# Kernel optimization log

Measured on AMD Instinct MI355X. Metric: run time of the kernel, lower is better.

The kernel has to match this reference:

```python
import jax, jax.numpy as jnp
import numpy as np

# structural constants (from dg config / init_kwargs)
B = 8192      # batch (L=1)
N = 64        # number of columns
C = 16        # one-hot width per column
D = N * C     # 1024
NUM = 32      # first NUM columns are numeric (use info['range'])
NCAUSAL = 16  # causal_cols = range(16)
K = 8         # info['range'][i] is [C, K]
HS = 1024
HP = 1024
TAU = 0.7
SMOOTH = 0.1  # kwargs['smoothing']


def setup_inputs() -> dict:
    key = jax.random.key(0)
    ks = jax.random.split(key, 20)
    s = 0.02
    inp = {
        'x': jax.random.uniform(ks[0], (B, D), dtype=jnp.float32),
        'truth_x': jax.random.normal(ks[1], (B, N), dtype=jnp.float32),
        # selector: Linear(D,HS) -> ReLU -> Linear(HS,N) -> Sigmoid
        'sel_w1': jax.random.normal(ks[2], (D, HS)) * s,
        'sel_b1': jnp.zeros((HS,), jnp.float32),
        'sel_w2': jax.random.normal(ks[3], (HS, N)) * s,
        'sel_b2': jnp.zeros((N,), jnp.float32),
        # perturber: D->HP->HP->HP->D with ReLU between
        'pw1': jax.random.normal(ks[4], (D, HP)) * s,
        'pb1': jnp.zeros((HP,), jnp.float32),
        'pw2': jax.random.normal(ks[5], (HP, HP)) * s,
        'pb2': jnp.zeros((HP,), jnp.float32),
        'pw3': jax.random.normal(ks[6], (HP, HP)) * s,
        'pb3': jnp.zeros((HP,), jnp.float32),
        'pw4': jax.random.normal(ks[7], (HP, D)) * s,
        'pb4': jnp.zeros((D,), jnp.float32),
        # dg.info['range'][i] for numeric columns: [NUM, C, K]
        'ranges': jax.random.normal(ks[8], (NUM, C, K), dtype=jnp.float32),
        # pre-drawn noise (training branch)
        'unif_a': jax.random.uniform(ks[9], (B, N), minval=1e-6, maxval=1.0 - 1e-6),
        'unif_b': jax.random.uniform(ks[10], (B, N), minval=1e-6, maxval=1.0 - 1e-6),
        'gumbel': jax.random.gumbel(ks[11], (B, N, C), dtype=jnp.float32),
    }
    return inp


def reference(x, truth_x, sel_w1, sel_b1, sel_w2, sel_b2,
              pw1, pb1, pw2, pb2, pw3, pb3, pw4, pb4,
              ranges, unif_a, unif_b, gumbel):
    # selector -> P in (0,1), shape [B, N]
    P = jax.nn.sigmoid(jax.nn.relu(x @ sel_w1 + sel_b1) @ sel_w2 + sel_b2)
    # relaxed Bernoulli (Sample_Bernoulli, training branch)
    ga = -jnp.log(-jnp.log(unif_a))
    gb = -jnp.log(-jnp.log(unif_b))
    no_logits = P * jnp.exp(ga) / TAU
    de_logits = no_logits + (1.0 - P) * jnp.exp(gb) / TAU
    probs = no_logits / de_logits                       # [B, N]
    # perturber MLP -> W, shape [B, D]
    h = jax.nn.relu(x @ pw1 + pb1)
    h = jax.nn.relu(h @ pw2 + pb2)
    h = jax.nn.relu(h @ pw3 + pb3)
    W = h @ pw4 + pb4
    # per-column blocks
    xr = x.reshape(B, N, C)
    logits = W.reshape(B, N, C)
    # data-dependent causal masking for causal columns
    curr = jnp.argmax(xr, axis=-1)                      # [B, N]
    causal = (jnp.arange(N) < NCAUSAL)[None, :, None]   # [1, N, 1]
    below = jnp.arange(C)[None, None, :] < curr[:, :, None]
    mask = jnp.where(causal & below, -100.0, jnp.where(causal, 1.0, 0.0))
    logits = logits + mask
    # label smoothing then Gumbel-softmax (soft), per Sample_Categorical
    pr = jax.nn.softmax(logits, axis=-1)
    pr = (1.0 - SMOOTH) * pr + SMOOTH / C
    logits = jnp.log(pr)
    y = jax.nn.softmax((logits + gumbel) / TAU, axis=-1)  # [B, N, C]
    # numeric columns: map categorical sample through range table, mix with truth
    xt_num = jnp.einsum('bnc,nck->bnk', y[:, :NUM], ranges).mean(axis=-1)  # [B, NUM]
    p_num = probs[:, :NUM]
    out_num = p_num * xt_num + (1.0 - p_num) * truth_x[:, :NUM]           # [B, NUM]
    # categorical columns: mix relaxed sample with original one-hot block
    p_cat = probs[:, NUM:, None]
    out_cat = p_cat * y[:, NUM:] + (1.0 - p_cat) * xr[:, NUM:]            # [B, N-NUM, C]
    xcf = jnp.concatenate([out_num, out_cat.reshape(B, (N - NUM) * C)], axis=1)
    return truth_x, xcf, P, W
```

## Files before the change

### kernel.cpp

```cpp
#include <hip/hip_runtime.h>
#include <hip/hip_bf16.h>
#include <cstdint>

#define B_DIM 8192
#define N_DIM 64
#define C_DIM 16
#define D_DIM 1024
#define NUM 32
#define NCAUSAL 16
#define K_RANGES 8
#define HS 1024
#define HP 1024
#define TAU 0.7f
#define SMOOTH 0.1f

typedef __bf16 bf16x8 __attribute__((ext_vector_type(8)));
typedef float f32x16 __attribute__((ext_vector_type(16)));

typedef const __attribute__((address_space(1))) uint32_t* gas_ptr;
typedef __attribute__((address_space(3))) uint32_t* las_ptr;

__device__ __forceinline__ void gld_lds16(const void* g, void* l) {
    __builtin_amdgcn_global_load_lds((gas_ptr)(uintptr_t)g,
                                     (las_ptr)(uint32_t)(uintptr_t)l,
                                     16, 0, 0);
}

__device__ __forceinline__ int swz(int r) { return (r & 3) ^ ((r >> 2) & 3); }

__device__ __forceinline__ void xcd_remap(int& bx, int& by)
{
    int gx  = gridDim.x;
    int nwg = gx * gridDim.y;
    int lin = by * gx + bx;
    int cpx = nwg >> 3;
    int sw  = (lin & 7) * cpx + (lin >> 3);
    by = sw / gx;
    bx = sw - by * gx;
}

template <int ACT>
__device__ __forceinline__ void gemm_body8(
    const ushort* __restrict__ Ag, const ushort* __restrict__ Bg,
    const float* __restrict__ bias,
    float* __restrict__ Cf, __hip_bfloat16* __restrict__ Cb,
    int lda, int Nout, int ldC, int K, long m0, long n0,
    uint4 (*As)[512], uint4 (*Bs)[512], f32x16* accExp = nullptr)
{
    const int tid  = threadIdx.x;
    const int wave = tid >> 6;
    const int ln31 = tid & 31, blk = (tid >> 5) & 1;
    const int wr = wave >> 2, wc = wave & 3;

    const int row = tid >> 2;
    const int ch  = (tid & 3) ^ swz(row);
    const ushort* aSrc = Ag + (m0 + row) * (long)lda + ch * 8;
    const ushort* bSrc = Bg + (n0 + row) * (long)K   + ch * 8;
    const int ldsOff = wave << 6;

    f32x16 acc[2];
    acc[0] = (f32x16)(0.0f);
    acc[1] = (f32x16)(0.0f);

#define ISSUE_STAGE8(buf, kt)                                                  \
    {                                                                          \
        gld_lds16(aSrc + (kt), &As[buf][ldsOff]);                              \
        gld_lds16(bSrc + (kt), &Bs[buf][ldsOff]);                              \
    }

    const int nt = K >> 5;
    ISSUE_STAGE8(0, 0);
    ISSUE_STAGE8(1, 32);

    int rb = 0;
    for (int t = 0; t < nt; ++t) {
        if (t < nt - 1) {
            asm volatile("s_waitcnt vmcnt(2)" ::: "memory");
        } else {
            asm volatile("s_waitcnt vmcnt(0)" ::: "memory");
        }
        __builtin_amdgcn_s_barrier();

        if (t + 2 < nt) {
            int sb = rb + 2; if (sb >= 3) sb -= 3;
            ISSUE_STAGE8(sb, (t + 2) * 32);
        }

        bf16x8 af[2][2], bfr[2];
#pragma unroll
        for (int ks = 0; ks < 2; ++ks) {
            int c = ks * 2 + blk;
#pragma unroll
            for (int mi = 0; mi < 2; ++mi) {
                int r = wr * 64 + mi * 32 + ln31;
                af[ks][mi] = __builtin_bit_cast(bf16x8, As[rb][r * 4 + (c ^ swz(r))]);
            }
            int n = wc * 32 + ln31;
            bfr[ks] = __builtin_bit_cast(bf16x8, Bs[rb][n * 4 + (c ^ swz(n))]);
        }
#pragma unroll
        for (int ks = 0; ks < 2; ++ks)
#pragma unroll
            for (int mi = 0; mi < 2; ++mi)
                acc[mi] = __builtin_amdgcn_mfma_f32_32x32x16_bf16(
                    af[ks][mi], bfr[ks], acc[mi], 0, 0, 0);

        rb = (rb == 2) ? 0 : rb + 1;
    }
#undef ISSUE_STAGE8

    if (ACT == 3) { accExp[0] = acc[0]; accExp[1] = acc[1]; }

    long col = n0 + wc * 32 + ln31;
    if (col < Nout) {
        float bs = bias ? bias[col] : 0.0f;
#pragma unroll
        for (int mi = 0; mi < 2; ++mi) {
#pragma unroll
            for (int reg = 0; reg < 16; ++reg) {
                long r2 = m0 + wr * 64 + mi * 32 + (reg & 3) + 8 * (reg >> 2) + 4 * blk;
                float v = acc[mi][reg] + bs;
                if (ACT == 1) {
                    v = fmaxf(v, 0.0f);
                    Cb[r2 * (long)ldC + col] = __float2bfloat16(v);
                } else if (ACT == 2) {
                    v = 1.0f / (1.0f + __expf(-v));
                    Cf[r2 * (long)ldC + col] = v;
                } else {
                    Cf[r2 * (long)ldC + col] = v;
                }
            }
        }
    }
}

template <int ACT>
__global__ __launch_bounds__(512, 4) void gemm8(
    const __hip_bfloat16* __restrict__ A, const __hip_bfloat16* __restrict__ Bt,
    const float* __restrict__ bias,
    float* __restrict__ Cf, __hip_bfloat16* __restrict__ Cb,
    int lda, int Nout, int ldC, int K)
{
    __shared__ uint4 As[3][512];
    __shared__ uint4 Bs[3][512];
    int bx = blockIdx.x, by = blockIdx.y;
    xcd_remap(bx, by);
    gemm_body8<ACT>((const ushort*)A, (const ushort*)Bt, bias, Cf, Cb,
                    lda, Nout, ldC, K,
                    (long)by * 128, (long)bx * 128, As, Bs);
}

__global__ __launch_bounds__(512, 4) void gemm8_fused23(
    const __hip_bfloat16* __restrict__ act1,
    const __hip_bfloat16* __restrict__ p2t, const float* __restrict__ pb2,
    __hip_bfloat16* __restrict__ actB,
    const __hip_bfloat16* __restrict__ w2t, const float* __restrict__ sel_b2,
    float* __restrict__ outP)
{
    __shared__ uint4 As[3][512];
    __shared__ uint4 Bs[3][512];
    int bx = blockIdx.x, by = blockIdx.y;
    xcd_remap(bx, by);
    long m0 = (long)by * 128;
    if (bx < 8) {
        gemm_body8<1>((const ushort*)(act1 + 1024), (const ushort*)p2t, pb2,
                      nullptr, actB, 2048, 1024, 1024, 1024,
                      m0, (long)bx * 128, As, Bs);
    } else {
        gemm_body8<2>((const ushort*)act1, (const ushort*)w2t, sel_b2,
                      outP, nullptr, 2048, 64, 64, 1024,
                      m0, 0, As, Bs);
    }
}

struct FinArgs {
    const float* x; const float* truth; const float* ua; const float* ub;
    const float* gum; const float* rmean; const float* P;
    float* out_truth; float* out_xcf;
};

__global__ __launch_bounds__(512, 4) void gemm8_final(
    const __hip_bfloat16* __restrict__ A, const __hip_bfloat16* __restrict__ Bt,
    const float* __restrict__ bias, float* __restrict__ W,
    int lda, int K, FinArgs fa)
{
    __shared__ uint4 smem[3072];
    uint4 (*As)[512] = reinterpret_cast<uint4(*)[512]>(smem);
    uint4 (*Bs)[512] = reinterpret_cast<uint4(*)[512]>(smem + 1536);

    int bx = blockIdx.x, by = blockIdx.y;
    xcd_remap(bx, by);
    const long m0 = (long)by * 128;
    const long n0 = (long)bx * 128;

    f32x16 accE[2];
    gemm_body8<3>((const ushort*)A, (const ushort*)Bt, bias, W, nullptr,
                  lda, 1024, 1024, K, m0, n0, As, Bs, accE);

    const int tid  = threadIdx.x;
    const int wave = tid >> 6;
    const int ln31 = tid & 31, blk = (tid >> 5) & 1;
    const int wr = wave >> 2, wc = wave & 3;

    float* tile = (float*)smem;
    const float bs = bias[n0 + wc * 32 + ln31];

    const int lb = tid >> 3;
    const int ng = tid & 7;
    const int n  = (int)(n0 >> 4) + ng;

    for (int h = 0; h < 2; ++h) {
        __syncthreads();
        if (wr == h) {
#pragma unroll
            for (int mi = 0; mi < 2; ++mi)
#pragma unroll
                for (int reg = 0; reg < 16; ++reg) {
                    int lr = mi * 32 + (reg & 3) + 8 * (reg >> 2) + 4 * blk;
                    tile[lr * 132 + wc * 32 + ln31] = accE[mi][reg] + bs;
                }
        }
        __syncthreads();

        long b   = m0 + h * 64 + lb;
        long idx = b * 64 + n;

        float tx = fa.truth[idx];
        fa.out_truth[idx] = tx;

        float p  = fa.P[idx];
        float ea = -1.0f / logf(fa.ua[idx]);
        float eb = -1.0f / logf(fa.ub[idx]);
        float no = p * ea;
        float probs = no / (no + (1.0f - p) * eb);

        const float* Wrow = tile + lb * 132 + ng * 16;
        const float* grow = fa.gum + (size_t)idx * 16;
        float lo[16], g[16], xv[16];
#pragma unroll
        for (int c = 0; c < 16; c += 4) {
            float4 v = *(const float4*)(Wrow + c);
            lo[c] = v.x; lo[c + 1] = v.y; lo[c + 2] = v.z; lo[c + 3] = v.w;
            float4 gv = *(const float4*)(grow + c);
            g[c] = gv.x; g[c + 1] = gv.y; g[c + 2] = gv.z; g[c + 3] = gv.w;
        }

        bool needx = (n < NCAUSAL) || (n >= NUM);
        if (needx) {
            const float* xrow = fa.x + (size_t)idx * 16;
#pragma unroll
            for (int c = 0; c < 16; c += 4) {
                float4 v = *(const float4*)(xrow + c);
                xv[c] = v.x; xv[c + 1] = v.y; xv[c + 2] = v.z; xv[c + 3] = v.w;
            }
        }

        if (n < NCAUSAL) {
            int curr = 0; float best = xv[0];
#pragma unroll
            for (int c = 1; c < 16; ++c)
                if (xv[c] > best) { best = xv[c]; curr = c; }
#pragma unroll
            for (int c = 0; c < 16; ++c) lo[c] += (c < curr) ? -100.0f : 1.0f;
        }

        float mx = lo[0];
#pragma unroll
        for (int c = 1; c < 16; ++c) mx = fmaxf(mx, lo[c]);
        float s = 0.0f, pr[16];
#pragma unroll
        for (int c = 0; c < 16; ++c) { pr[c] = __expf(lo[c] - mx); s += pr[c]; }
        float inv = 1.0f / s;
#pragma unroll
        for (int c = 0; c < 16; ++c)
            pr[c] = (1.0f - SMOOTH) * pr[c] * inv + (SMOOTH / C_DIM);

        float t[16];
        float mx2 = -1e30f;
#pragma unroll
        for (int c = 0; c < 16; ++c) {
            t[c] = (__logf(pr[c]) + g[c]) * (1.0f / TAU);
            mx2 = fmaxf(mx2, t[c]);
        }
        float s2 = 0.0f;
#pragma unroll
        for (int c = 0; c < 16; ++c) { t[c] = __expf(t[c] - mx2); s2 += t[c]; }
        float inv2 = 1.0f / s2;

        if (n < NUM) {
            float xt = 0.0f;
#pragma unroll
            for (int c = 0; c < 16; ++c) xt += t[c] * inv2 * fa.rmean[n * 16 + c];
            fa.out_xcf[(size_t)b * 544 + n] = probs * xt + (1.0f - probs) * tx;
        } else {
            float* o = fa.out_xcf + (size_t)b * 544 + 32 + (size_t)(n - NUM) * 16;
#pragma unroll
            for (int c = 0; c < 16; ++c)
                o[c] = probs * t[c] * inv2 + (1.0f - probs) * xv[c];
        }
    }
}

struct PrepArgs {
    const float* src[6];
    __hip_bfloat16* dst[6];
    int Nsrc[6];
    int Npad[6];
    const float* ranges; float* rmean;
    const float* b1; const float* b2; float* bcat;
    const float* x; __hip_bfloat16* xbf;
};

__global__ void prep_kernel(PrepArgs a)
{
    int z = blockIdx.z;
    int tx = threadIdx.x, ty = threadIdx.y;
    int t = ty * 32 + tx;
    if (z == 7) {
        int bid = blockIdx.y * 32 + blockIdx.x;
        const float4* s4 = (const float4*)a.x;
        for (int i = bid * 256 + t; i < B_DIM * D_DIM / 4; i += 1024 * 256) {
            float4 v = s4[i];
            __hip_bfloat16* d = a.xbf + (size_t)i * 4;
            d[0] = __float2bfloat16(v.x);
            d[1] = __float2bfloat16(v.y);
            d[2] = __float2bfloat16(v.z);
            d[3] = __float2bfloat16(v.w);
        }
        return;
    }
    if (z == 6) {
        if (blockIdx.x || blockIdx.y) return;
        for (int j = t; j < NUM * C_DIM; j += 256) {
            float s = 0.0f;
#pragma unroll
            for (int k = 0; k < K_RANGES; ++k) s += a.ranges[j * K_RANGES + k];
            a.rmean[j] = s * (1.0f / K_RANGES);
        }
        for (int j = t; j < 1024; j += 256) {
            a.bcat[j]        = a.b1[j];
            a.bcat[1024 + j] = a.b2[j];
        }
        return;
    }
    const int Nsrc = a.Nsrc[z], Npad = a.Npad[z];
    int n0 = blockIdx.x * 32, k0 = blockIdx.y * 32;
    if (n0 >= Npad) return;
    const float* src = a.src[z];
    __hip_bfloat16* dst = a.dst[z];
    __shared__ float tile[32][33];
#pragma unroll
    for (int i = 0; i < 32; i += 8) {
        int k = k0 + ty + i, n = n0 + tx;
        tile[ty + i][tx] = (n < Nsrc) ? src[(size_t)k * Nsrc + n] : 0.0f;
    }
    __syncthreads();
#pragma unroll
    for (int i = 0; i < 32; i += 8) {
        int n = n0 + ty + i, k = k0 + tx;
        dst[(size_t)n * D_DIM + k] = __float2bfloat16(tile[tx][ty + i]);
    }
}

extern "C" void kernel_launch(void* const* d_in, const int* in_sizes, int n_in,
                              void* d_out, int out_size, void* d_ws, size_t ws_size,
                              hipStream_t stream)
{
    const float* x      = (const float*)d_in[0];
    const float* truth  = (const float*)d_in[1];
    const float* sel_w1 = (const float*)d_in[2];
    const float* sel_b1 = (const float*)d_in[3];
    const float* sel_w2 = (const float*)d_in[4];
    const float* sel_b2 = (const float*)d_in[5];
    const float* pw1    = (const float*)d_in[6];
    const float* pb1    = (const float*)d_in[7];
    const float* pw2    = (const float*)d_in[8];
    const float* pb2    = (const float*)d_in[9];
    const float* pw3    = (const float*)d_in[10];
    const float* pb3    = (const float*)d_in[11];
    const float* pw4    = (const float*)d_in[12];
    const float* pb4    = (const float*)d_in[13];
    const float* ranges = (const float*)d_in[14];
    const float* ua     = (const float*)d_in[15];
    const float* ub     = (const float*)d_in[16];
    const float* gum    = (const float*)d_in[17];

    float* out       = (float*)d_out;
    float* out_truth = out;
    float* out_xcf   = out + 524288;
    float* out_P     = out + 4980736;
    float* out_W     = out + 5505024;

    char* w = (char*)d_ws;
    size_t off = 0;
    __hip_bfloat16* A0   = (__hip_bfloat16*)(w + off); off += (size_t)B_DIM * D_DIM * 2;
    __hip_bfloat16* act1 = (__hip_bfloat16*)(w + off); off += (size_t)B_DIM * 2048 * 2;
    __hip_bfloat16* actB = (__hip_bfloat16*)(w + off); off += (size_t)B_DIM * HP * 2;
    __hip_bfloat16* actC = (__hip_bfloat16*)(w + off); off += (size_t)B_DIM * HP * 2;
    __hip_bfloat16* Wcat = (__hip_bfloat16*)(w + off); off += (size_t)2048 * D_DIM * 2;
    __hip_bfloat16* w2t  = (__hip_bfloat16*)(w + off); off += (size_t)128 * HS * 2;
    __hip_bfloat16* p2t  = (__hip_bfloat16*)(w + off); off += (size_t)HP * HP * 2;
    __hip_bfloat16* p3t  = (__hip_bfloat16*)(w + off); off += (size_t)HP * HP * 2;
    __hip_bfloat16* p4t  = (__hip_bfloat16*)(w + off); off += (size_t)D_DIM * HP * 2;
    float* rmean         = (float*)(w + off);          off += 512 * 4;
    float* bcat          = (float*)(w + off);          off += 2048 * 4;
    if (ws_size < off) return;

    PrepArgs pa;
    pa.src[0] = sel_w1; pa.dst[0] = Wcat;               pa.Nsrc[0] = HS;    pa.Npad[0] = 1024;
    pa.src[1] = pw1;    pa.dst[1] = Wcat + 1024 * 1024; pa.Nsrc[1] = HP;    pa.Npad[1] = 1024;
    pa.src[2] = sel_w2; pa.dst[2] = w2t;                pa.Nsrc[2] = N_DIM; pa.Npad[2] = 128;
    pa.src[3] = pw2;    pa.dst[3] = p2t;                pa.Nsrc[3] = HP;    pa.Npad[3] = 1024;
    pa.src[4] = pw3;    pa.dst[4] = p3t;                pa.Nsrc[4] = HP;    pa.Npad[4] = 1024;
    pa.src[5] = pw4;    pa.dst[5] = p4t;                pa.Nsrc[5] = D_DIM; pa.Npad[5] = 1024;
    pa.ranges = ranges; pa.rmean = rmean;
    pa.b1 = sel_b1; pa.b2 = pb1; pa.bcat = bcat;
    pa.x = x; pa.xbf = A0;

    prep_kernel<<<dim3(32, 32, 8), dim3(32, 8), 0, stream>>>(pa);

    gemm8<1><<<dim3(16, 64), 512, 0, stream>>>(A0, Wcat, bcat, nullptr, act1,
                                               D_DIM, 2048, 2048, D_DIM);
    gemm8_fused23<<<dim3(9, 64), 512, 0, stream>>>(act1, p2t, pb2, actB, w2t,
                                                   sel_b2, out_P);
    gemm8<1><<<dim3(8, 64), 512, 0, stream>>>(actB, p3t, pb3, nullptr, actC,
                                              HP, HP, HP, HP);
    FinArgs fa;
    fa.x = x; fa.truth = truth; fa.ua = ua; fa.ub = ub; fa.gum = gum;
    fa.rmean = rmean; fa.P = out_P;
    fa.out_truth = out_truth; fa.out_xcf = out_xcf;
    gemm8_final<<<dim3(8, 64), 512, 0, stream>>>(actC, p4t, pb4, out_W,
                                                 HP, HP, fa);
}
```

Before: 300.3 us.

## Use 4-wave double-buffered GEMM with 2x2 MFMA tiles for first layer

```diff
diff --git a/kernel.cpp b/kernel.cpp
--- a/kernel.cpp
+++ b/kernel.cpp
@@ -37,6 +37,123 @@
     int sw  = (lin & 7) * cpx + (lin >> 3);
     by = sw / gx;
     bx = sw - by * gx;
+}
+
+template <int ACT>
+__device__ __forceinline__ void gemm_body2(
+    const ushort* __restrict__ Ag, const ushort* __restrict__ Bg,
+    const float* __restrict__ bias,
+    float* __restrict__ Cf, __hip_bfloat16* __restrict__ Cb,
+    int lda, int Nout, int ldC, int K, long m0, long n0,
+    uint4 (*As)[512], uint4 (*Bs)[512])
+{
+    const int tid  = threadIdx.x;
+    const int wave = tid >> 6;
+    const int lane = tid & 63;
+    const int wr = wave >> 1, wc = wave & 1;
+    const int ln31 = lane & 31, blk = lane >> 5;
+
+    f32x16 acc[2][2];
+#pragma unroll
+    for (int i = 0; i < 2; ++i)
+#pragma unroll
+        for (int j = 0; j < 2; ++j) acc[i][j] = (f32x16)(0.0f);
+
+    const int c0 = wave * 128 + lane;
+    const int c1 = wave * 128 + 64 + lane;
+
+#define ISSUE_STAGE2(buf, kt)                                                  \
+    {                                                                          \
+        int r0 = c0 >> 2, kc0 = (c0 & 3) ^ swz(r0);                            \
+        int r1 = c1 >> 2, kc1 = (c1 & 3) ^ swz(r1);                            \
+        gld_lds16(Ag + (m0 + r0) * (long)lda + (kt) + kc0 * 8,                 \
+                  &As[buf][wave * 128]);                                       \
+        gld_lds16(Bg + (n0 + r0) * (long)K + (kt) + kc0 * 8,                   \
+                  &Bs[buf][wave * 128]);                                       \
+        gld_lds16(Ag + (m0 + r1) * (long)lda + (kt) + kc1 * 8,                 \
+                  &As[buf][wave * 128 + 64]);                                  \
+        gld_lds16(Bg + (n0 + r1) * (long)K + (kt) + kc1 * 8,                   \
+                  &Bs[buf][wave * 128 + 64]);                                  \
+    }
+
+    ISSUE_STAGE2(0, 0);
+    int cur = 0;
+    for (int kt = 0; kt < K; kt += 32) {
+        __syncthreads();
+        if (kt + 32 < K) ISSUE_STAGE2(cur ^ 1, kt + 32);
+
+        bf16x8 af[2][2], bfr[2][2];
+#pragma unroll
+        for (int ks = 0; ks < 2; ++ks) {
+            int ch = ks * 2 + blk;
+#pragma unroll
+            for (int mi = 0; mi < 2; ++mi) {
+                int r = wr * 64 + mi * 32 + ln31;
+                af[ks][mi] = __builtin_bit_cast(bf16x8, As[cur][r * 4 + (ch ^ swz(r))]);
+            }
+#pragma unroll
+            for (int ni = 0; ni < 2; ++ni) {
+                int n = wc * 64 + ni * 32 + ln31;
+                bfr[ks][ni] = __builtin_bit_cast(bf16x8, Bs[cur][n * 4 + (ch ^ swz(n))]);
+            }
+        }
+#pragma unroll
+        for (int ks = 0; ks < 2; ++ks)
+#pragma unroll
+            for (int mi = 0; mi < 2; ++mi)
+#pragma unroll
+                for (int ni = 0; ni < 2; ++ni)
+                    acc[mi][ni] = __builtin_amdgcn_mfma_f32_32x32x16_bf16(
+                        af[ks][mi], bfr[ks][ni], acc[mi][ni], 0, 0, 0);
+        cur ^= 1;
+    }
+#undef ISSUE_STAGE2
+
+    float bs2[2];
+#pragma unroll
+    for (int ni = 0; ni < 2; ++ni) {
+        long col = n0 + wc * 64 + ni * 32 + ln31;
+        bs2[ni] = (col < Nout && bias) ? bias[col] : 0.0f;
+    }
+
+#pragma unroll
+    for (int mi = 0; mi < 2; ++mi) {
+#pragma unroll
+        for (int ni = 0; ni < 2; ++ni) {
+            long col = n0 + wc * 64 + ni * 32 + ln31;
+            if (col >= Nout) continue;
+#pragma unroll
+            for (int reg = 0; reg < 16; ++reg) {
+                long row = m0 + wr * 64 + mi * 32 + (reg & 3) + 8 * (reg >> 2) + 4 * blk;
+                float v = acc[mi][ni][reg] + bs2[ni];
+                if (ACT == 1) {
+                    v = fmaxf(v, 0.0f);
+                    Cb[row * (long)ldC + col] = __float2bfloat16(v);
+                } else if (ACT == 2) {
+                    v = 1.0f / (1.0f + __expf(-v));
+                    Cf[row * (long)ldC + col] = v;
+                } else {
+                    Cf[row * (long)ldC + col] = v;
+                }
+            }
+        }
+    }
+}
+
+template <int ACT>
+__global__ __launch_bounds__(256, 4) void gemm2(
+    const __hip_bfloat16* __restrict__ A, const __hip_bfloat16* __restrict__ Bt,
+    const float* __restrict__ bias,
+    float* __restrict__ Cf, __hip_bfloat16* __restrict__ Cb,
+    int lda, int Nout, int ldC, int K)
+{
+    __shared__ uint4 As[2][512];
+    __shared__ uint4 Bs[2][512];
+    int bx = blockIdx.x, by = blockIdx.y;
+    xcd_remap(bx, by);
+    gemm_body2<ACT>((const ushort*)A, (const ushort*)Bt, bias, Cf, Cb,
+                    lda, Nout, ldC, K,
+                    (long)by * 128, (long)bx * 128, As, Bs);
 }
 
 template <int ACT>
@@ -134,22 +251,6 @@
     }
 }
 
-template <int ACT>
-__global__ __launch_bounds__(512, 4) void gemm8(
-    const __hip_bfloat16* __restrict__ A, const __hip_bfloat16* __restrict__ Bt,
-    const float* __restrict__ bias,
-    float* __restrict__ Cf, __hip_bfloat16* __restrict__ Cb,
-    int lda, int Nout, int ldC, int K)
-{
-    __shared__ uint4 As[3][512];
-    __shared__ uint4 Bs[3][512];
-    int bx = blockIdx.x, by = blockIdx.y;
-    xcd_remap(bx, by);
-    gemm_body8<ACT>((const ushort*)A, (const ushort*)Bt, bias, Cf, Cb,
-                    lda, Nout, ldC, K,
-                    (long)by * 128, (long)bx * 128, As, Bs);
-}
-
 __global__ __launch_bounds__(512, 4) void gemm8_fused23(
     const __hip_bfloat16* __restrict__ act1,
     const __hip_bfloat16* __restrict__ p2t, const float* __restrict__ pb2,
@@ -171,6 +272,22 @@
                       outP, nullptr, 2048, 64, 64, 1024,
                       m0, 0, As, Bs);
     }
+}
+
+template <int ACT>
+__global__ __launch_bounds__(512, 4) void gemm8(
+    const __hip_bfloat16* __restrict__ A, const __hip_bfloat16* __restrict__ Bt,
+    const float* __restrict__ bias,
+    float* __restrict__ Cf, __hip_bfloat16* __restrict__ Cb,
+    int lda, int Nout, int ldC, int K)
+{
+    __shared__ uint4 As[3][512];
+    __shared__ uint4 Bs[3][512];
+    int bx = blockIdx.x, by = blockIdx.y;
+    xcd_remap(bx, by);
+    gemm_body8<ACT>((const ushort*)A, (const ushort*)Bt, bias, Cf, Cb,
+                    lda, Nout, ldC, K,
+                    (long)by * 128, (long)bx * 128, As, Bs);
 }
 
 struct FinArgs {
@@ -419,7 +536,7 @@
 
     prep_kernel<<<dim3(32, 32, 8), dim3(32, 8), 0, stream>>>(pa);
 
-    gemm8<1><<<dim3(16, 64), 512, 0, stream>>>(A0, Wcat, bcat, nullptr, act1,
+    gemm2<1><<<dim3(16, 64), 256, 0, stream>>>(A0, Wcat, bcat, nullptr, act1,
                                                D_DIM, 2048, 2048, D_DIM);
     gemm8_fused23<<<dim3(9, 64), 512, 0, stream>>>(act1, p2t, pb2, actB, w2t,
                                                    sel_b2, out_P);
```

After: 304.1 us. No clear change (+1.3%).
